# Kernel tuning notes

Measured on AMD Instinct MI355X. Metric: run time of the kernel, lower is better.

The kernel has to match this reference:

```python
import jax, jax.numpy as jnp
import numpy as np

DEGREE = 3          # bspline_array passes t_dim positionally as degree
C_DIM = 64          # coefficients per spline
N_SPLINES = 64      # n
T_DIM = C_DIM + DEGREE + 1   # knots per spline = 68
BATCH = 65536


def setup_inputs() -> dict:
    key = jax.random.key(0)
    k1, k2, k3 = jax.random.split(key, 3)
    x = jax.random.normal(k1, (BATCH, N_SPLINES), dtype=jnp.float32)
    t = jax.random.normal(k2, (N_SPLINES, T_DIM), dtype=jnp.float32)   # knot vectors (learned, unsorted as in source)
    c = jax.random.normal(k3, (N_SPLINES, C_DIM), dtype=jnp.float32)   # control coefficients
    return {"x": x, "t": t, "c": c}


def _safe_div(num, den):
    # Cox-de Boor convention: 0/0 := 0 (handles repeated knots)
    zero = den == 0
    return jnp.where(zero, 0.0, num / jnp.where(zero, 1.0, den))


def cox_deboor_batched(t, c, x):
    """Vectorized Cox-de Boor over all n splines and the whole batch.

    t: [n, T_DIM] knots, c: [n, C_DIM] coeffs, x: [B, n] -> out [B, n]
    """
    xe = x[..., None]                                   # [B, n, 1]
    # degree-0 basis: indicator t_i <= x < t_{i+1}      # [B, n, T_DIM-1]
    N = ((t[:, :-1] <= xe) & (xe < t[:, 1:])).astype(x.dtype)
    for k in range(1, DEGREE + 1):
        m = T_DIM - 1 - k
        left = _safe_div(xe - t[:, :m], t[:, k:k + m] - t[:, :m]) * N[..., :m]
        right = _safe_div(t[:, k + 1:k + 1 + m] - xe,
                          t[:, k + 1:k + 1 + m] - t[:, 1:1 + m]) * N[..., 1:1 + m]
        N = left + right                                # [B, n, m]
    # S(x) = sum_i c_i * B_{i,p}(x)
    return jnp.einsum('bni,ni->bn', N[..., :C_DIM], c)  # [B, n]


def reference(x, t, c):
    return cox_deboor_batched(t, c, x)
```

## Files before the change

kernel.cpp:

```cpp
#include <hip/hip_runtime.h>

#define BATCH 65536
#define NSPL  64
#define CDIM  64
#define TDIM  68
#define QI    67
#define RTN   67

#define TCOLS 16
#define TROWS 128
#define NTHR  256
#define PITCH 129


__global__ __launch_bounds__(128) void prep(const float* __restrict__ T,
                                            const float* __restrict__ C,
                                            float4* __restrict__ RT) {
    __shared__ double  td[TDIM];
    __shared__ double  cd[CDIM];
    __shared__ double  R1[QI], R2[TDIM - 2], R3[TDIM - 3];
    __shared__ double4 Qd[QI];
    __shared__ float   tf[TDIM];
    __shared__ float   srt[TDIM];

    const int s = blockIdx.x;
    const int t = threadIdx.x;

    if (t < TDIM) { float v = T[s * TDIM + t]; tf[t] = v; td[t] = (double)v; }
    if (t >= 64 && t < 64 + CDIM) cd[t - 64] = (double)C[s * CDIM + t - 64];
    __syncthreads();

    if (t < TDIM - 1) { double d = td[t + 1] - td[t]; R1[t] = (d == 0.0) ? 0.0 : 1.0 / d; }
    if (t < TDIM - 2) { double d = td[t + 2] - td[t]; R2[t] = (d == 0.0) ? 0.0 : 1.0 / d; }
    if (t < TDIM - 3) { double d = td[t + 3] - td[t]; R3[t] = (d == 0.0) ? 0.0 : 1.0 / d; }
    if (t < TDIM) {
        float v = tf[t];
        int r = 0;
        for (int k = 0; k < TDIM; ++k)
            r += (tf[k] < v) || (tf[k] == v && k < t);
        srt[r] = v;
    }
    __syncthreads();

    if (t < QI) {
        const int i = t;
        double q0 = 0, q1 = 0, q2 = 0, q3 = 0;
        for (int j = i - 3; j <= i; ++j) {
            if (j < 0 || j > CDIM - 1) continue;
            double cj = cd[j];
            for (int b2 = 0; b2 < 2; ++b2) {
                int m2 = j + b2;
                double D3 = R3[j + b2];
                double p3 = b2 ? -D3 : D3;
                double r3 = b2 ? D3 * td[j + 4] : -D3 * td[j];
                for (int b1 = 0; b1 < 2; ++b1) {
                    int m1 = m2 + b1;
                    double D2 = R2[m2 + b1];
                    double p2 = b1 ? -D2 : D2;
                    double r2 = b1 ? D2 * td[m2 + 3] : -D2 * td[m2];
                    for (int b0 = 0; b0 < 2; ++b0) {
                        if (m1 + b0 != i) continue;
                        double D1 = R1[m1 + b0];
                        double p1 = b0 ? -D1 : D1;
                        double r1 = b0 ? D1 * td[m1 + 2] : -D1 * td[m1];
                        double a2 = p3 * p2, a1 = p3 * r2 + r3 * p2, a0 = r3 * r2;
                        q3 += cj * (a2 * p1);
                        q2 += cj * (a2 * r1 + a1 * p1);
                        q1 += cj * (a1 * r1 + a0 * p1);
                        q0 += cj * (a0 * r1);
                    }
                }
            }
        }
        double4 q; q.x = q0; q.y = q1; q.z = q2; q.w = q3;
        Qd[i] = q;
    }
    __syncthreads();

    if (t >= 1 && t <= RTN) {
        const float xs = srt[t - 1];
        double a0 = 0, a1 = 0, a2 = 0, a3 = 0;
        for (int i = 0; i < QI; ++i) {
            if (tf[i] <= xs && xs < tf[i + 1]) {
                double4 q = Qd[i];
                a0 += q.x; a1 += q.y; a2 += q.z; a3 += q.w;
            }
        }
        float4 v; v.x = (float)a0; v.y = (float)a1; v.z = (float)a2; v.w = (float)a3;
        RT[s * RTN + (t - 1)] = v;
    }
}

__global__ __launch_bounds__(NTHR) void bspline_main(const float* __restrict__ X,
                                                     const float* __restrict__ T,
                                                     const float4* __restrict__ RT,
                                                     float* __restrict__ O) {
    __shared__ float xl[TCOLS * PITCH];

    const int tid  = threadIdx.x;
    const int lane = tid & 63;
    const int w    = tid >> 6;
    const int r0   = blockIdx.x * TROWS;
    const int s0   = blockIdx.y * TCOLS;

    #pragma unroll
    for (int it = 0; it < TROWS * TCOLS / NTHR; ++it) {
        int e = tid + it * NTHR;
        int r = e >> 4, c = e & 15;
        xl[c * PITCH + r] = X[(r0 + r) * NSPL + s0 + c];
    }
    __syncthreads();

    #pragma unroll 1
    for (int cc = 0; cc < 4; ++cc) {
        const int c  = w * 4 + cc;
        const int sp = __builtin_amdgcn_readfirstlane(s0 + c);
        const float* kn = T + sp * TDIM;

        float* xc = xl + c * PITCH + lane;
        const float x0 = xc[0];
        const float x1 = xc[64];
        unsigned n0 = 0, n1 = 0;
        #pragma unroll
        for (int j = 0; j < TDIM; ++j) {
            float tj = kn[j];
            n0 += (x0 >= tj);
            n1 += (x1 >= tj);
        }
        unsigned i0 = n0 - 1u; i0 = (i0 > 66u) ? 66u : i0;
        unsigned i1 = n1 - 1u; i1 = (i1 > 66u) ? 66u : i1;
        const float4* rts = RT + sp * RTN;
        float4 p0 = rts[i0];
        float4 p1 = rts[i1];
        float y0 = fmaf(fmaf(fmaf(p0.w, x0, p0.z), x0, p0.y), x0, p0.x);
        float y1 = fmaf(fmaf(fmaf(p1.w, x1, p1.z), x1, p1.y), x1, p1.x);
        y0 = (n0 - 1u < 67u) ? y0 : 0.f;
        y1 = (n1 - 1u < 67u) ? y1 : 0.f;
        xc[0]  = y0;
        xc[64] = y1;
    }
    __syncthreads();

    #pragma unroll
    for (int it = 0; it < TROWS * TCOLS / NTHR; ++it) {
        int e = tid + it * NTHR;
        int r = e >> 4, c = e & 15;
        O[(r0 + r) * NSPL + s0 + c] = xl[c * PITCH + r];
    }
}

extern "C" void kernel_launch(void* const* d_in, const int* in_sizes, int n_in,
                              void* d_out, int out_size, void* d_ws, size_t ws_size,
                              hipStream_t stream) {
    const float* X = (const float*)d_in[0];
    const float* T = (const float*)d_in[1];
    const float* C = (const float*)d_in[2];
    float* O = (float*)d_out;
    float4* RT = (float4*)d_ws;

    prep<<<NSPL, 128, 0, stream>>>(T, C, RT);
    dim3 grid(BATCH / TROWS, NSPL / TCOLS);
    bspline_main<<<grid, NTHR, 0, stream>>>(X, T, RT, O);
}
```

Baseline: 100.9 us.

## Binary-search sorted knots in LDS and vectorize X/O tile transfers

```diff
diff --git a/kernel.cpp b/kernel.cpp
--- a/kernel.cpp
+++ b/kernel.cpp
@@ -11,11 +11,13 @@
 #define TROWS 128
 #define NTHR  256
 #define PITCH 129
+#define KPAD  128
 
 
 __global__ __launch_bounds__(128) void prep(const float* __restrict__ T,
                                             const float* __restrict__ C,
-                                            float4* __restrict__ RT) {
+                                            float4* __restrict__ RT,
+                                            float* __restrict__ SRT) {
     __shared__ double  td[TDIM];
     __shared__ double  cd[CDIM];
     __shared__ double  R1[QI], R2[TDIM - 2], R3[TDIM - 3];
@@ -41,6 +43,11 @@
         srt[r] = v;
     }
     __syncthreads();
+
+    {
+        float v = (t < TDIM) ? srt[t] : __builtin_huge_valf();
+        SRT[s * KPAD + t] = v;
+    }
 
     if (t < QI) {
         const int i = t;
@@ -92,10 +99,11 @@
 }
 
 __global__ __launch_bounds__(NTHR) void bspline_main(const float* __restrict__ X,
-                                                     const float* __restrict__ T,
                                                      const float4* __restrict__ RT,
+                                                     const float* __restrict__ SRT,
                                                      float* __restrict__ O) {
     __shared__ float xl[TCOLS * PITCH];
+    __shared__ float ks[TCOLS * KPAD];
 
     const int tid  = threadIdx.x;
     const int lane = tid & 63;
@@ -103,11 +111,21 @@
     const int r0   = blockIdx.x * TROWS;
     const int s0   = blockIdx.y * TCOLS;
 
+    {
+        const float4* src = (const float4*)(SRT + s0 * KPAD);
+        float4* dst = (float4*)ks;
+        dst[tid]        = src[tid];
+        dst[tid + NTHR] = src[tid + NTHR];
+    }
     #pragma unroll
-    for (int it = 0; it < TROWS * TCOLS / NTHR; ++it) {
+    for (int it = 0; it < 2; ++it) {
         int e = tid + it * NTHR;
-        int r = e >> 4, c = e & 15;
-        xl[c * PITCH + r] = X[(r0 + r) * NSPL + s0 + c];
+        int r = e >> 2, q = e & 3;
+        float4 v = *(const float4*)(X + (r0 + r) * NSPL + s0 + q * 4);
+        xl[(q * 4 + 0) * PITCH + r] = v.x;
+        xl[(q * 4 + 1) * PITCH + r] = v.y;
+        xl[(q * 4 + 2) * PITCH + r] = v.z;
+        xl[(q * 4 + 3) * PITCH + r] = v.w;
     }
     __syncthreads();
 
@@ -115,17 +133,19 @@
     for (int cc = 0; cc < 4; ++cc) {
         const int c  = w * 4 + cc;
         const int sp = __builtin_amdgcn_readfirstlane(s0 + c);
-        const float* kn = T + sp * TDIM;
+        const float* kc = ks + c * KPAD;
 
         float* xc = xl + c * PITCH + lane;
         const float x0 = xc[0];
         const float x1 = xc[64];
+
         unsigned n0 = 0, n1 = 0;
         #pragma unroll
-        for (int j = 0; j < TDIM; ++j) {
-            float tj = kn[j];
-            n0 += (x0 >= tj);
-            n1 += (x1 >= tj);
+        for (int st = 64; st >= 1; st >>= 1) {
+            float v0 = kc[n0 + st - 1];
+            float v1 = kc[n1 + st - 1];
+            n0 = (v0 <= x0) ? n0 + st : n0;
+            n1 = (v1 <= x1) ? n1 + st : n1;
         }
         unsigned i0 = n0 - 1u; i0 = (i0 > 66u) ? 66u : i0;
         unsigned i1 = n1 - 1u; i1 = (i1 > 66u) ? 66u : i1;
@@ -142,10 +162,15 @@
     __syncthreads();
 
     #pragma unroll
-    for (int it = 0; it < TROWS * TCOLS / NTHR; ++it) {
+    for (int it = 0; it < 2; ++it) {
         int e = tid + it * NTHR;
-        int r = e >> 4, c = e & 15;
-        O[(r0 + r) * NSPL + s0 + c] = xl[c * PITCH + r];
+        int r = e >> 2, q = e & 3;
+        float4 v;
+        v.x = xl[(q * 4 + 0) * PITCH + r];
+        v.y = xl[(q * 4 + 1) * PITCH + r];
+        v.z = xl[(q * 4 + 2) * PITCH + r];
+        v.w = xl[(q * 4 + 3) * PITCH + r];
+        *(float4*)(O + (r0 + r) * NSPL + s0 + q * 4) = v;
     }
 }
 
@@ -157,8 +182,9 @@
     const float* C = (const float*)d_in[2];
     float* O = (float*)d_out;
     float4* RT = (float4*)d_ws;
+    float* SRT = (float*)((char*)d_ws + NSPL * RTN * sizeof(float4));
 
-    prep<<<NSPL, 128, 0, stream>>>(T, C, RT);
+    prep<<<NSPL, 128, 0, stream>>>(T, C, RT, SRT);
     dim3 grid(BATCH / TROWS, NSPL / TCOLS);
-    bspline_main<<<grid, NTHR, 0, stream>>>(X, T, RT, O);
+    bspline_main<<<grid, NTHR, 0, stream>>>(X, RT, SRT, O);
 }
```

New measurement: 88.83 us. 1.14x faster.
